# Kernel optimization log

Measured on AMD Instinct MI355X. Metric: run time of the kernel, lower is better.

## Reference

```python
import jax, jax.numpy as jnp
import numpy as np

B, F, T, C = 2, 4, 1024, 1536   # batch, features, ticks, channels
NW = [476, 476, 292]            # wires per plane (same layout for both faces)
NX = 1536                       # wire crossings per face


def _make_wc(rng, nw, nchan):
    # rows: (wire_ident, channel); idents form a permutation of [0, nw)
    ident = rng.permutation(nw)
    chan = rng.integers(0, nchan, size=nw)
    return jnp.asarray(np.stack([ident, chan], axis=1), dtype=jnp.int32)


def setup_inputs() -> dict:
    key = jax.random.key(0)
    rng = np.random.default_rng(0)
    x = jax.random.normal(key, (B, F, T, C), dtype=jnp.float32)
    wcs = {f"wc{i}{j}": _make_wc(rng, NW[j], C) for i in range(2) for j in range(3)}
    xms = {f"xm{i}": jnp.asarray(
        np.stack([rng.integers(0, NW[j], size=NX) for j in range(3)], axis=1),
        dtype=jnp.int32) for i in range(2)}
    w_seg = jax.random.normal(jax.random.fold_in(key, 1), (1, F), dtype=jnp.float32) * 0.1
    b_seg = jnp.zeros((1,), dtype=jnp.float32)
    return {"x": x, **wcs, **xms, "w_seg": w_seg, "b_seg": b_seg}


def _face(x, wcs_face, xm):
    # x: (B,F,T,C); wcs_face: list of 3 (nw,2) int maps; xm: (NX,3)
    outs = []
    for j in range(3):
        ident, chan = wcs_face[j][:, 0], wcs_face[j][:, 1]
        nw = wcs_face[j].shape[0]
        # gather channels, reindex into wire order (scatter-set by wire ident)
        wsv = jnp.zeros(x.shape[:-1] + (nw,), x.dtype).at[..., ident].set(x[..., chan])
        idx = xm[:, j]                                  # (NX,)
        gathered = wsv[..., idx]                        # (B,F,T,NX); crossover term == identity
        # segment-mean back onto wires: scatter_add + count + clamp(min=1)
        summed = jnp.zeros_like(wsv).at[..., idx].add(gathered)
        cnt = jnp.zeros((nw,), x.dtype).at[idx].add(1.0)
        summed = summed / jnp.clip(cnt, 1.0, None)
        outs.append((summed, chan))
    return outs


def reference(x, wc00, wc01, wc02, wc10, wc11, wc12, xm0, xm1, w_seg, b_seg):
    wcs = [[wc00, wc01, wc02], [wc10, wc11, wc12]]
    xms = [xm0, xm1]
    nchan = x.shape[-1]
    y = jnp.zeros_like(x)                # (B,F,T,C)
    cy = jnp.zeros((nchan,), x.dtype)
    for i in range(2):
        for summed, chan in _face(x, wcs[i], xms[i]):
            y = y.at[..., chan].add(summed)   # scatter-add wire terms onto channels
            cy = cy.at[chan].add(1.0)
    y = y / jnp.clip(cy, 1.0, None)
    y = jnp.transpose(y, (0, 1, 3, 2))        # (B,F,C,T)
    logits = jnp.einsum('bfct,of->boct', y, w_seg) + b_seg[None, :, None, None]
    return jax.nn.sigmoid(logits)             # (B,1,C,T)
```

## Files before the change

kernel.cpp:

```cpp
#include <hip/hip_runtime.h>

#define B_ 2
#define F_ 4
#define T_ 1024
#define C_ 1536
#define NX_ 1536
#define CAP 64
#define TILE 64
#define ZT_BLOCKS ((T_ / TILE) * (C_ / TILE) * B_)

struct MetaSh {
    int masks[4096];
    int cnt[C_];
    int cy[C_];
};

union SharedU {
    float tile[TILE][TILE + 1];
    MetaSh m;
};

__global__ __launch_bounds__(256) void zt_meta(
    const float* __restrict__ x, const float* __restrict__ w_seg,
    float* __restrict__ zT,
    const int* __restrict__ wc00, const int* __restrict__ wc01, const int* __restrict__ wc02,
    const int* __restrict__ wc10, const int* __restrict__ wc11, const int* __restrict__ wc12,
    const int* __restrict__ xm0, const int* __restrict__ xm1,
    int nw0, int nw1, int nw2,
    int* __restrict__ count,
    int* __restrict__ edges,
    float* __restrict__ scale)
{
    __shared__ SharedU sh;
    const int tid = threadIdx.x;

    if (blockIdx.x == ZT_BLOCKS) {
        const int* wcs[6] = {wc00, wc01, wc02, wc10, wc11, wc12};
        const int* xms[2] = {xm0, xm1};
        int nws[3] = {nw0, nw1, nw2};
        int moff[6];
        int tot = 0;
        for (int f = 0; f < 6; ++f) { moff[f] = tot; tot += nws[f % 3]; }

        for (int s = tid; s < 4096; s += 256) sh.m.masks[s] = 0;
        for (int c = tid; c < C_; c += 256) { sh.m.cnt[c] = 0; sh.m.cy[c] = 0; }
        __syncthreads();

        for (int i = 0; i < 2; ++i)
            for (int j = 0; j < 3; ++j) {
                const int f = i * 3 + j;
                const int* xm = xms[i];
                for (int p = tid; p < NX_; p += 256)
                    sh.m.masks[moff[f] + xm[p * 3 + j]] = 1;
            }
        __syncthreads();

        for (int f = 0; f < 6; ++f) {
            const int nw = nws[f % 3];
            const int* wc = wcs[f];
            for (int k = tid; k < nw; k += 256) {
                const int src = wc[k * 2 + 1];
                atomicAdd(&sh.m.cy[src], 1);
                const int s = wc[k * 2 + 0];
                if (sh.m.masks[moff[f] + s]) {
                    const int dst = wc[s * 2 + 1];
                    const int pos = atomicAdd(&sh.m.cnt[dst], 1);
                    if (pos < CAP) edges[dst * CAP + pos] = src;
                }
            }
        }
        __syncthreads();

        for (int c = tid; c < C_; c += 256) {
            count[c] = sh.m.cnt[c];
            const int cv = sh.m.cy[c];
            scale[c] = 1.0f / (float)(cv > 0 ? cv : 1);
        }
        return;
    }

    const int bid  = blockIdx.x;
    const int tpb  = T_ / TILE;
    const int b    = bid / (tpb * (C_ / TILE));
    const int rem  = bid % (tpb * (C_ / TILE));
    const int t0   = (rem % tpb) * TILE;
    const int c0   = (rem / tpb) * TILE;

    const int lo = tid & 15;
    const int hi = tid >> 4;

    const float w0 = w_seg[0], w1 = w_seg[1], w2 = w_seg[2], w3 = w_seg[3];
    const float* xb = x + (size_t)b * F_ * T_ * C_;
    const size_t fs = (size_t)T_ * C_;

    #pragma unroll
    for (int p = 0; p < 4; ++p) {
        const int tt = p * 16 + hi;
        const size_t base = (size_t)(t0 + tt) * C_ + c0 + lo * 4;
        const float4 a0 = *reinterpret_cast<const float4*>(xb + base);
        const float4 a1 = *reinterpret_cast<const float4*>(xb + base + fs);
        const float4 a2 = *reinterpret_cast<const float4*>(xb + base + 2 * fs);
        const float4 a3 = *reinterpret_cast<const float4*>(xb + base + 3 * fs);
        sh.tile[tt][lo * 4 + 0] = w0 * a0.x + w1 * a1.x + w2 * a2.x + w3 * a3.x;
        sh.tile[tt][lo * 4 + 1] = w0 * a0.y + w1 * a1.y + w2 * a2.y + w3 * a3.y;
        sh.tile[tt][lo * 4 + 2] = w0 * a0.z + w1 * a1.z + w2 * a2.z + w3 * a3.z;
        sh.tile[tt][lo * 4 + 3] = w0 * a0.w + w1 * a1.w + w2 * a2.w + w3 * a3.w;
    }
    __syncthreads();

    float* zb = zT + (size_t)b * C_ * T_;
    #pragma unroll
    for (int p = 0; p < 4; ++p) {
        const int cr = p * 16 + hi;
        const int t4 = lo * 4;
        float4 o;
        o.x = sh.tile[t4 + 0][cr];
        o.y = sh.tile[t4 + 1][cr];
        o.z = sh.tile[t4 + 2][cr];
        o.w = sh.tile[t4 + 3][cr];
        *reinterpret_cast<float4*>(zb + (size_t)(c0 + cr) * T_ + t0 + t4) = o;
    }
}

__global__ __launch_bounds__(256) void gather_out(
    const float* __restrict__ zT,
    const int* __restrict__ edges, const int* __restrict__ count,
    const float* __restrict__ scale, const float* __restrict__ b_seg,
    float* __restrict__ out)
{
    const int c = blockIdx.x;
    const int b = blockIdx.y;
    const int n = min(count[c], CAP);
    const float sc = scale[c];
    const float bs = b_seg[0];

    const float* zb = zT + (size_t)b * C_ * T_;
    const int t = threadIdx.x * 4;

    float4 acc = make_float4(0.f, 0.f, 0.f, 0.f);
    for (int e = 0; e < n; ++e) {
        const int src = edges[c * CAP + e];
        const float4 v = *reinterpret_cast<const float4*>(zb + (size_t)src * T_ + t);
        acc.x += v.x; acc.y += v.y; acc.z += v.z; acc.w += v.w;
    }
    float4 o;
    o.x = 1.f / (1.f + expf(-(acc.x * sc + bs)));
    o.y = 1.f / (1.f + expf(-(acc.y * sc + bs)));
    o.z = 1.f / (1.f + expf(-(acc.z * sc + bs)));
    o.w = 1.f / (1.f + expf(-(acc.w * sc + bs)));
    *reinterpret_cast<float4*>(out + ((size_t)b * C_ + c) * T_ + t) = o;
}

extern "C" void kernel_launch(void* const* d_in, const int* in_sizes, int n_in,
                              void* d_out, int out_size, void* d_ws, size_t ws_size,
                              hipStream_t stream) {
    const float* x     = (const float*)d_in[0];
    const int* wc00    = (const int*)d_in[1];
    const int* wc01    = (const int*)d_in[2];
    const int* wc02    = (const int*)d_in[3];
    const int* wc10    = (const int*)d_in[4];
    const int* wc11    = (const int*)d_in[5];
    const int* wc12    = (const int*)d_in[6];
    const int* xm0     = (const int*)d_in[7];
    const int* xm1     = (const int*)d_in[8];
    const float* w_seg = (const float*)d_in[9];
    const float* b_seg = (const float*)d_in[10];
    float* out         = (float*)d_out;

    const int nw0 = in_sizes[1] / 2;
    const int nw1 = in_sizes[2] / 2;
    const int nw2 = in_sizes[3] / 2;

    char* ws = (char*)d_ws;
    size_t off = 0;
    float* zT    = (float*)(ws + off); off += (size_t)B_ * C_ * T_ * sizeof(float);
    int* edges   = (int*)(ws + off);   off += (size_t)C_ * CAP * sizeof(int);
    int* count   = (int*)(ws + off);   off += (size_t)C_ * sizeof(int);
    float* scale = (float*)(ws + off); off += (size_t)C_ * sizeof(float);

    zt_meta<<<ZT_BLOCKS + 1, 256, 0, stream>>>(
        x, w_seg, zT,
        wc00, wc01, wc02, wc10, wc11, wc12,
        xm0, xm1, nw0, nw1, nw2,
        count, edges, scale);

    gather_out<<<dim3(C_, B_), 256, 0, stream>>>(zT, edges, count, scale, b_seg, out);
}
```

Baseline: 120.7 us.

## Fuse projection, edge-list build and gather into one LDS-resident kernel

Two launches become one kernel. Each block owns a 16-tick slice of one batch. It projects the four features into a shared-memory tile over all channels, rebuilds the channel edge lists locally (bitmask, ushort edges, CAP lowered to 12) and then gathers, averages and applies the sigmoid straight from shared memory. This removes the global zT intermediate, its write and re-read, and the second launch. In exchange, every block repeats the metadata construction, the grid is only 128 blocks of 1024 threads using about 147KB of LDS, and any channel with more than 12 incoming edges would be silently truncated.

```diff
diff --git a/kernel.cpp b/kernel.cpp
--- a/kernel.cpp
+++ b/kernel.cpp
@@ -5,150 +5,112 @@
 #define T_ 1024
 #define C_ 1536
 #define NX_ 1536
-#define CAP 64
-#define TILE 64
-#define ZT_BLOCKS ((T_ / TILE) * (C_ / TILE) * B_)
+#define CAP 12
+#define TT 16
+#define ZPAD 1540
+#define NBLK ((T_ / TT) * B_)
 
-struct MetaSh {
-    int masks[4096];
-    int cnt[C_];
-    int cy[C_];
-};
+__device__ __forceinline__ float sigmoidf_(float v) {
+    return 1.0f / (1.0f + __expf(-v));
+}
 
-union SharedU {
-    float tile[TILE][TILE + 1];
-    MetaSh m;
-};
-
-__global__ __launch_bounds__(256) void zt_meta(
+__global__ __launch_bounds__(1024) void fused_kernel(
     const float* __restrict__ x, const float* __restrict__ w_seg,
-    float* __restrict__ zT,
+    const float* __restrict__ b_seg,
     const int* __restrict__ wc00, const int* __restrict__ wc01, const int* __restrict__ wc02,
     const int* __restrict__ wc10, const int* __restrict__ wc11, const int* __restrict__ wc12,
     const int* __restrict__ xm0, const int* __restrict__ xm1,
     int nw0, int nw1, int nw2,
-    int* __restrict__ count,
-    int* __restrict__ edges,
-    float* __restrict__ scale)
+    float* __restrict__ out)
 {
-    __shared__ SharedU sh;
+    __shared__ float z[TT][ZPAD];
+    __shared__ int cy[C_];
+    __shared__ int cnt[C_];
+    __shared__ unsigned short edges[C_][CAP];
+    __shared__ unsigned int mask[16];
     const int tid = threadIdx.x;
-
-    if (blockIdx.x == ZT_BLOCKS) {
-        const int* wcs[6] = {wc00, wc01, wc02, wc10, wc11, wc12};
-        const int* xms[2] = {xm0, xm1};
-        int nws[3] = {nw0, nw1, nw2};
-        int moff[6];
-        int tot = 0;
-        for (int f = 0; f < 6; ++f) { moff[f] = tot; tot += nws[f % 3]; }
-
-        for (int s = tid; s < 4096; s += 256) sh.m.masks[s] = 0;
-        for (int c = tid; c < C_; c += 256) { sh.m.cnt[c] = 0; sh.m.cy[c] = 0; }
-        __syncthreads();
-
-        for (int i = 0; i < 2; ++i)
-            for (int j = 0; j < 3; ++j) {
-                const int f = i * 3 + j;
-                const int* xm = xms[i];
-                for (int p = tid; p < NX_; p += 256)
-                    sh.m.masks[moff[f] + xm[p * 3 + j]] = 1;
-            }
-        __syncthreads();
-
-        for (int f = 0; f < 6; ++f) {
-            const int nw = nws[f % 3];
-            const int* wc = wcs[f];
-            for (int k = tid; k < nw; k += 256) {
-                const int src = wc[k * 2 + 1];
-                atomicAdd(&sh.m.cy[src], 1);
-                const int s = wc[k * 2 + 0];
-                if (sh.m.masks[moff[f] + s]) {
-                    const int dst = wc[s * 2 + 1];
-                    const int pos = atomicAdd(&sh.m.cnt[dst], 1);
-                    if (pos < CAP) edges[dst * CAP + pos] = src;
-                }
-            }
-        }
-        __syncthreads();
-
-        for (int c = tid; c < C_; c += 256) {
-            count[c] = sh.m.cnt[c];
-            const int cv = sh.m.cy[c];
-            scale[c] = 1.0f / (float)(cv > 0 ? cv : 1);
-        }
-        return;
-    }
-
-    const int bid  = blockIdx.x;
-    const int tpb  = T_ / TILE;
-    const int b    = bid / (tpb * (C_ / TILE));
-    const int rem  = bid % (tpb * (C_ / TILE));
-    const int t0   = (rem % tpb) * TILE;
-    const int c0   = (rem / tpb) * TILE;
-
-    const int lo = tid & 15;
-    const int hi = tid >> 4;
+    const int b   = blockIdx.x / (T_ / TT);
+    const int t0  = (blockIdx.x % (T_ / TT)) * TT;
 
     const float w0 = w_seg[0], w1 = w_seg[1], w2 = w_seg[2], w3 = w_seg[3];
     const float* xb = x + (size_t)b * F_ * T_ * C_;
     const size_t fs = (size_t)T_ * C_;
 
     #pragma unroll
-    for (int p = 0; p < 4; ++p) {
-        const int tt = p * 16 + hi;
-        const size_t base = (size_t)(t0 + tt) * C_ + c0 + lo * 4;
+    for (int it = 0; it < 6; ++it) {
+        const int idx = tid + it * 1024;
+        const int tt  = idx / 384;
+        const int cq  = idx - tt * 384;
+        const size_t base = (size_t)(t0 + tt) * C_ + cq * 4;
         const float4 a0 = *reinterpret_cast<const float4*>(xb + base);
         const float4 a1 = *reinterpret_cast<const float4*>(xb + base + fs);
         const float4 a2 = *reinterpret_cast<const float4*>(xb + base + 2 * fs);
         const float4 a3 = *reinterpret_cast<const float4*>(xb + base + 3 * fs);
-        sh.tile[tt][lo * 4 + 0] = w0 * a0.x + w1 * a1.x + w2 * a2.x + w3 * a3.x;
-        sh.tile[tt][lo * 4 + 1] = w0 * a0.y + w1 * a1.y + w2 * a2.y + w3 * a3.y;
-        sh.tile[tt][lo * 4 + 2] = w0 * a0.z + w1 * a1.z + w2 * a2.z + w3 * a3.z;
-        sh.tile[tt][lo * 4 + 3] = w0 * a0.w + w1 * a1.w + w2 * a2.w + w3 * a3.w;
+        float4 zv;
+        zv.x = w0 * a0.x + w1 * a1.x + w2 * a2.x + w3 * a3.x;
+        zv.y = w0 * a0.y + w1 * a1.y + w2 * a2.y + w3 * a3.y;
+        zv.z = w0 * a0.z + w1 * a1.z + w2 * a2.z + w3 * a3.z;
+        zv.w = w0 * a0.w + w1 * a1.w + w2 * a2.w + w3 * a3.w;
+        *reinterpret_cast<float4*>(&z[tt][cq * 4]) = zv;
     }
+    for (int c = tid; c < C_; c += 1024) { cy[c] = 0; cnt[c] = 0; }
     __syncthreads();
 
-    float* zb = zT + (size_t)b * C_ * T_;
+    const int* wcs[6] = {wc00, wc01, wc02, wc10, wc11, wc12};
+    const int* xms[2] = {xm0, xm1};
+    const int nws[3]  = {nw0, nw1, nw2};
+
+    for (int f = 0; f < 6; ++f) {
+        if (tid < 16) mask[tid] = 0u;
+        __syncthreads();
+        const int jj = f % 3;
+        const int* xm = xms[f / 3];
+        for (int p = tid; p < NX_; p += 1024) {
+            const int s = xm[p * 3 + jj];
+            atomicOr(&mask[s >> 5], 1u << (s & 31));
+        }
+        __syncthreads();
+        const int nw = nws[jj];
+        const int* wc = wcs[f];
+        for (int k = tid; k < nw; k += 1024) {
+            const int s    = wc[k * 2 + 0];
+            const int srcc = wc[k * 2 + 1];
+            atomicAdd(&cy[srcc], 1);
+            if ((mask[s >> 5] >> (s & 31)) & 1u) {
+                const int dst = wc[s * 2 + 1];
+                const int pos = atomicAdd(&cnt[dst], 1);
+                if (pos < CAP) edges[dst][pos] = (unsigned short)srcc;
+            }
+        }
+        __syncthreads();
+    }
+
+    const float bs = b_seg[0];
+    float* ob = out + (size_t)b * C_ * T_;
+
     #pragma unroll
-    for (int p = 0; p < 4; ++p) {
-        const int cr = p * 16 + hi;
-        const int t4 = lo * 4;
+    for (int it = 0; it < 6; ++it) {
+        const int idx = tid + it * 1024;
+        const int c   = idx >> 2;
+        const int tq  = idx & 3;
+        const int n   = min(cnt[c], CAP);
+        const float inv = 1.0f / (float)max(cy[c], 1);
+        const int tb = tq * 4;
+        float4 acc = make_float4(0.f, 0.f, 0.f, 0.f);
+        for (int e = 0; e < n; ++e) {
+            const int src = edges[c][e];
+            acc.x += z[tb + 0][src];
+            acc.y += z[tb + 1][src];
+            acc.z += z[tb + 2][src];
+            acc.w += z[tb + 3][src];
+        }
         float4 o;
-        o.x = sh.tile[t4 + 0][cr];
-        o.y = sh.tile[t4 + 1][cr];
-        o.z = sh.tile[t4 + 2][cr];
-        o.w = sh.tile[t4 + 3][cr];
-        *reinterpret_cast<float4*>(zb + (size_t)(c0 + cr) * T_ + t0 + t4) = o;
+        o.x = sigmoidf_(acc.x * inv + bs);
+        o.y = sigmoidf_(acc.y * inv + bs);
+        o.z = sigmoidf_(acc.z * inv + bs);
+        o.w = sigmoidf_(acc.w * inv + bs);
+        *reinterpret_cast<float4*>(&ob[(size_t)c * T_ + t0 + tb]) = o;
     }
-}
-
-__global__ __launch_bounds__(256) void gather_out(
-    const float* __restrict__ zT,
-    const int* __restrict__ edges, const int* __restrict__ count,
-    const float* __restrict__ scale, const float* __restrict__ b_seg,
-    float* __restrict__ out)
-{
-    const int c = blockIdx.x;
-    const int b = blockIdx.y;
-    const int n = min(count[c], CAP);
-    const float sc = scale[c];
-    const float bs = b_seg[0];
-
-    const float* zb = zT + (size_t)b * C_ * T_;
-    const int t = threadIdx.x * 4;
-
-    float4 acc = make_float4(0.f, 0.f, 0.f, 0.f);
-    for (int e = 0; e < n; ++e) {
-        const int src = edges[c * CAP + e];
-        const float4 v = *reinterpret_cast<const float4*>(zb + (size_t)src * T_ + t);
-        acc.x += v.x; acc.y += v.y; acc.z += v.z; acc.w += v.w;
-    }
-    float4 o;
-    o.x = 1.f / (1.f + expf(-(acc.x * sc + bs)));
-    o.y = 1.f / (1.f + expf(-(acc.y * sc + bs)));
-    o.z = 1.f / (1.f + expf(-(acc.z * sc + bs)));
-    o.w = 1.f / (1.f + expf(-(acc.w * sc + bs)));
-    *reinterpret_cast<float4*>(out + ((size_t)b * C_ + c) * T_ + t) = o;
 }
 
 extern "C" void kernel_launch(void* const* d_in, const int* in_sizes, int n_in,
@@ -171,18 +133,9 @@
     const int nw1 = in_sizes[2] / 2;
     const int nw2 = in_sizes[3] / 2;
 
-    char* ws = (char*)d_ws;
-    size_t off = 0;
-    float* zT    = (float*)(ws + off); off += (size_t)B_ * C_ * T_ * sizeof(float);
-    int* edges   = (int*)(ws + off);   off += (size_t)C_ * CAP * sizeof(int);
-    int* count   = (int*)(ws + off);   off += (size_t)C_ * sizeof(int);
-    float* scale = (float*)(ws + off); off += (size_t)C_ * sizeof(float);
-
-    zt_meta<<<ZT_BLOCKS + 1, 256, 0, stream>>>(
-        x, w_seg, zT,
+    fused_kernel<<<NBLK, 1024, 0, stream>>>(
+        x, w_seg, b_seg,
         wc00, wc01, wc02, wc10, wc11, wc12,
         xm0, xm1, nw0, nw1, nw2,
-        count, edges, scale);
-
-    gather_out<<<dim3(C_, B_), 256, 0, stream>>>(zT, edges, count, scale, b_seg, out);
+        out);
 }
```

Result: faster. 115.9 us (-4.0%).
